# Optimization experiments

Measured on AMD Instinct MI355X. Metric: run time of the kernel, lower is better.

Reference implementation:

```python
import jax, jax.numpy as jnp
import numpy as np

B, C, T = 16, 256, 2048
K = 1024  # codes per layer
N_LAYERS = 3


def setup_inputs() -> dict:
    key = jax.random.key(0)
    kx, k0, k1, k2 = jax.random.split(key, 4)
    x = jax.random.normal(kx, (B, C, T), dtype=jnp.float32)
    scale = 1.0 / K
    emb0 = jax.random.uniform(k0, (K, C), minval=-scale, maxval=scale, dtype=jnp.float32)
    emb1 = jax.random.uniform(k1, (K, C), minval=-scale, maxval=scale, dtype=jnp.float32)
    emb2 = jax.random.uniform(k2, (K, C), minval=-scale, maxval=scale, dtype=jnp.float32)
    return {"x": x, "emb0": emb0, "emb1": emb1, "emb2": emb2}


def _vq_layer(x, emb):
    # x: [B, C, T], emb: [K, C]
    b, c, t = x.shape
    flat = jnp.transpose(x, (0, 2, 1)).reshape(-1, c)          # [B*T, C]
    # squared L2 distance to each code: ||f||^2 - 2 f.e + ||e||^2
    dist = (jnp.sum(flat * flat, axis=1, keepdims=True)
            - 2.0 * flat @ emb.T
            + jnp.sum(emb * emb, axis=1))                       # [B*T, K]
    idx = jnp.argmin(dist, axis=1)                              # [B*T]
    quant = jnp.transpose(emb[idx].reshape(b, t, c), (0, 2, 1)) # [B, C, T]
    sg = jax.lax.stop_gradient
    loss = jnp.mean((sg(quant) - x) ** 2) + jnp.mean((quant - sg(x)) ** 2)
    quantized = x + sg(quant - x)  # straight-through
    return quantized, loss


def reference(x, emb0, emb1, emb2):
    total_loss = jnp.float32(0.0)
    out = x
    for emb in (emb0, emb1, emb2):
        out, loss = _vq_layer(out, emb)
        total_loss = total_loss + loss
    return out, total_loss
```

## Files before the change

kernel.cpp:

```cpp
#include <hip/hip_runtime.h>
#include <stdint.h>

#define B_  16
#define C_  256
#define T_  2048
#define K_  1024
#define TOTAL_ELEMS 8388608

typedef short bf16x8 __attribute__((ext_vector_type(8)));
typedef float f32x4 __attribute__((ext_vector_type(4)));

__device__ __forceinline__ unsigned long long pack_key(float d, int idx) {
  unsigned u = __float_as_uint(d);
  u = (u & 0x80000000u) ? ~u : (u | 0x80000000u);
  return ((unsigned long long)u << 32) | (unsigned)idx;
}
__device__ __forceinline__ float unpack_dist(unsigned long long key) {
  unsigned du = (unsigned)(key >> 32);
  unsigned bits = (du & 0x80000000u) ? (du ^ 0x80000000u) : ~du;
  return __uint_as_float(bits);
}

__device__ __forceinline__ unsigned short f2bf_rne(float f) {
  unsigned u = __float_as_uint(f);
  unsigned r = u + 0x7FFFu + ((u >> 16) & 1u);
  return (unsigned short)(r >> 16);
}

__device__ __forceinline__ void gload_lds16(const void* g, void* l) {
  __builtin_amdgcn_global_load_lds(
      (const __attribute__((address_space(1))) unsigned int*)g,
      (__attribute__((address_space(3))) unsigned int*)l, 16, 0, 0);
}

__global__ __launch_bounds__(256) void prep_kernel(
    const float* __restrict__ e0, const float* __restrict__ e1,
    const float* __restrict__ e2, float* __restrict__ nrm,
    unsigned short* __restrict__ ebf) {
  int bid = blockIdx.x;
  if (bid < 12) {
    int i = bid * 256 + threadIdx.x;
    const float* e = (i < 1024) ? e0 : (i < 2048) ? e1 : e2;
    const float* p = e + (size_t)(i & 1023) * C_;
    float s = 0.0f;
    for (int c = 0; c < C_; c += 4) {
      float4 v = *(const float4*)(p + c);
      s = fmaf(v.x, v.x, s); s = fmaf(v.y, v.y, s);
      s = fmaf(v.z, v.z, s); s = fmaf(v.w, v.w, s);
    }
    nrm[i] = s;
  } else {
    int i = (bid - 12) * 256 + threadIdx.x;
    float4 v = *(const float4*)(e0 + (size_t)i * 4);
    unsigned lo = (unsigned)f2bf_rne(v.x) | ((unsigned)f2bf_rne(v.y) << 16);
    unsigned hi = (unsigned)f2bf_rne(v.z) | ((unsigned)f2bf_rne(v.w) << 16);
    *(uint2*)(ebf + (size_t)i * 4) = make_uint2(lo, hi);
  }
}

__global__ __launch_bounds__(256) void xpose_kernel(
    const float* __restrict__ x, unsigned short* __restrict__ xT) {
  __shared__ float ftile[64][68];
  int tid = threadIdx.x;
  int bid = blockIdx.x;
  int b  = bid >> 7;
  int t0 = ((bid >> 2) & 31) << 6;
  int c0 = (bid & 3) << 6;
  int w = tid >> 6, l = tid & 63;
  int c_loc = w * 16 + (l >> 4);
  int t_loc = (l & 15) * 4;
  const float* src = x + (size_t)b * (C_ * T_) + (size_t)(c0 + c_loc) * T_ + t0 + t_loc;
  float4 v = *(const float4*)src;
  *(float4*)&ftile[c_loc][t_loc] = v;
  __syncthreads();
  int t_row = tid >> 2;
  int cs = (tid & 3) * 16;
  unsigned pk[8];
#pragma unroll
  for (int i = 0; i < 8; i++) {
    unsigned short lo = f2bf_rne(ftile[cs + 2 * i][t_row]);
    unsigned short hi = f2bf_rne(ftile[cs + 2 * i + 1][t_row]);
    pk[i] = (unsigned)lo | ((unsigned)hi << 16);
  }
  unsigned short* dst = xT + ((size_t)(b * T_ + t0 + t_row) * C_ + c0 + cs);
  *(uint4*)dst       = make_uint4(pk[0], pk[1], pk[2], pk[3]);
  *((uint4*)dst + 1) = make_uint4(pk[4], pk[5], pk[6], pk[7]);
}

__global__ __launch_bounds__(256) void map_tile_kernel(
    const float* __restrict__ e0, const float* __restrict__ e1,
    const float* __restrict__ e2, const float* __restrict__ nrm,
    unsigned long long* __restrict__ keysM) {
  __shared__ float As[16][68];
  __shared__ float Bs[16][68];
  int bid = blockIdx.x;
  int m = bid >> 8;
  int tb = bid & 255;
  int ar0 = (tb >> 4) << 6;
  int br0 = (tb & 15) << 6;
  const float* Ap = m ? e1 : e0;
  const float* Bp = m ? e2 : e1;
  const float* nB = nrm + (m + 1) * 1024;

  int tid = threadIdx.x;
  int ty = tid >> 4, tx = tid & 15;
  int srow = tid >> 2;
  int skp  = (tid & 3) << 2;

  float acc[4][4];
#pragma unroll
  for (int i = 0; i < 4; i++)
#pragma unroll
    for (int j = 0; j < 4; j++) acc[i][j] = 0.0f;

  const float* gA = Ap + (size_t)(ar0 + srow) * C_ + skp;
  const float* gB = Bp + (size_t)(br0 + srow) * C_ + skp;

  for (int kk = 0; kk < C_; kk += 16) {
    float4 av = *(const float4*)(gA + kk);
    float4 bv = *(const float4*)(gB + kk);
    __syncthreads();
    As[skp + 0][srow] = av.x; As[skp + 1][srow] = av.y;
    As[skp + 2][srow] = av.z; As[skp + 3][srow] = av.w;
    Bs[skp + 0][srow] = bv.x; Bs[skp + 1][srow] = bv.y;
    Bs[skp + 2][srow] = bv.z; Bs[skp + 3][srow] = bv.w;
    __syncthreads();
#pragma unroll
    for (int k = 0; k < 16; k++) {
      float4 a4 = *(const float4*)&As[k][ty * 4];
      float4 b4 = *(const float4*)&Bs[k][tx * 4];
      float aa[4] = {a4.x, a4.y, a4.z, a4.w};
      float bb[4] = {b4.x, b4.y, b4.z, b4.w};
#pragma unroll
      for (int i = 0; i < 4; i++)
#pragma unroll
        for (int j = 0; j < 4; j++)
          acc[i][j] = fmaf(aa[i], bb[j], acc[i][j]);
    }
  }

  float nv[4];
#pragma unroll
  for (int j = 0; j < 4; j++) nv[j] = nB[br0 + tx * 4 + j];

#pragma unroll
  for (int i = 0; i < 4; i++) {
    unsigned long long best = 0xFFFFFFFFFFFFFFFFULL;
#pragma unroll
    for (int j = 0; j < 4; j++) {
      int code = br0 + tx * 4 + j;
      float s = nv[j] - 2.0f * acc[i][j];
      unsigned long long key = pack_key(s, code);
      if (key < best) best = key;
    }
#pragma unroll
    for (int off = 1; off < 16; off <<= 1) {
      unsigned long long o = __shfl_xor(best, off, 64);
      if (o < best) best = o;
    }
    if (tx == 0)
      atomicMin(&keysM[m * 1024 + ar0 + ty * 4 + i], best);
  }
}

__global__ __launch_bounds__(256) void l0_mfma_kernel(
    const unsigned short* __restrict__ xT, const unsigned short* __restrict__ ebf,
    const float* __restrict__ e0n, unsigned long long* __restrict__ keys) {
  __shared__ __align__(16) unsigned short AB[2][2][128][32];
  __shared__ unsigned long long kred[128][2];

  int tid = threadIdx.x;
  int l = tid & 63, w = tid >> 6;
  int wr = w >> 1, wc = w & 1;
  int mb = blockIdx.x & 255, nb = blockIdx.x >> 8;
  int row0 = mb << 7, kb = nb << 7;

  int sm = w * 32 + (l >> 2);
  int ks = (l & 3) ^ ((l >> 2) & 3);
  const unsigned short* gA = xT + ((size_t)(row0 + sm) * C_ + ks * 8);
  const unsigned short* gB = ebf + ((size_t)(kb + sm) * C_ + ks * 8);

  f32x4 acc[4][4];
#pragma unroll
  for (int mi = 0; mi < 4; mi++)
#pragma unroll
    for (int ni = 0; ni < 4; ni++) acc[mi][ni] = (f32x4){0.f, 0.f, 0.f, 0.f};

#define STAGE(buf, kk) do {                                              \
    char* baseA = (char*)&AB[(buf)][0][0][0] + w * 2048;                 \
    char* baseB = (char*)&AB[(buf)][1][0][0] + w * 2048;                 \
    gload_lds16(gA + (size_t)(kk) * 32, baseA);                          \
    gload_lds16(gA + (size_t)16 * C_ + (size_t)(kk) * 32, baseA + 1024); \
    gload_lds16(gB + (size_t)(kk) * 32, baseB);                          \
    gload_lds16(gB + (size_t)16 * C_ + (size_t)(kk) * 32, baseB + 1024); \
  } while (0)

  STAGE(0, 0);
  __syncthreads();

  int lr = l & 15, lg = l >> 4;
  int slot = lg ^ (lr & 3);
  int buf = 0;
  for (int kk = 0; kk < 8; kk++) {
    if (kk < 7) STAGE(buf ^ 1, kk + 1);
    bf16x8 aF[4], bF[4];
#pragma unroll
    for (int mi = 0; mi < 4; mi++)
      aF[mi] = *(const bf16x8*)&AB[buf][0][wr * 64 + mi * 16 + lr][slot * 8];
#pragma unroll
    for (int ni = 0; ni < 4; ni++)
      bF[ni] = *(const bf16x8*)&AB[buf][1][wc * 64 + ni * 16 + lr][slot * 8];
#pragma unroll
    for (int mi = 0; mi < 4; mi++)
#pragma unroll
      for (int ni = 0; ni < 4; ni++)
        acc[mi][ni] = __builtin_amdgcn_mfma_f32_16x16x32_bf16(
            aF[mi], bF[ni], acc[mi][ni], 0, 0, 0);
    __syncthreads();
    buf ^= 1;
  }
#undef STAGE

  float nv[4];
#pragma unroll
  for (int ni = 0; ni < 4; ni++) nv[ni] = e0n[kb + wc * 64 + ni * 16 + lr];

#pragma unroll
  for (int mi = 0; mi < 4; mi++) {
#pragma unroll
    for (int r = 0; r < 4; r++) {
      unsigned long long best = 0xFFFFFFFFFFFFFFFFULL;
#pragma unroll
      for (int ni = 0; ni < 4; ni++) {
        int code = kb + wc * 64 + ni * 16 + lr;
        float s = nv[ni] - 2.0f * acc[mi][ni][r];
        unsigned long long key = pack_key(s, code);
        if (key < best) best = key;
      }
#pragma unroll
      for (int off = 1; off < 16; off <<= 1) {
        unsigned long long o = __shfl_xor(best, off, 64);
        if (o < best) best = o;
      }
      if (lr == 0) kred[wr * 64 + mi * 16 + lg * 4 + r][wc] = best;
    }
  }
  __syncthreads();
  if (tid < 128) {
    unsigned long long b0 = kred[tid][0], b1 = kred[tid][1];
    atomicMin(&keys[row0 + tid], b0 < b1 ? b0 : b1);
  }
}

__global__ __launch_bounds__(256) void finish_kernel(
    const float* __restrict__ x, const float* __restrict__ emb2,
    const unsigned long long* __restrict__ keys,
    const unsigned long long* __restrict__ keysM,
    const float* __restrict__ nrm,
    float* __restrict__ out, float* __restrict__ loss_accum) {
  __shared__ int code2_l[64];
  __shared__ float rloss[64];
  __shared__ float fpart[4][64];
  int tid = threadIdx.x;
  int b  = blockIdx.x >> 5;
  int t0 = (blockIdx.x & 31) << 6;
  int tt = tid & 63, w = tid >> 6;

  if (w == 0) {
    unsigned long long key0 = keys[(size_t)b * T_ + t0 + tt];
    int idx0 = (int)(key0 & 0xFFFFFFFFULL);
    float s0 = unpack_dist(key0);
    unsigned long long k1 = keysM[idx0];
    int c1 = (int)(k1 & 0xFFFFFFFFULL);
    unsigned long long k2 = keysM[1024 + c1];
    code2_l[tt] = (int)(k2 & 0xFFFFFFFFULL);
    rloss[tt] = s0 + nrm[idx0] + unpack_dist(k1) + nrm[1024 + c1] + unpack_dist(k2);
  }
  __syncthreads();

  const float* xb = x + ((size_t)b << 19);
  float* ob = out + ((size_t)b << 19);
  int code2 = code2_l[tt];
  const float* e2row = emb2 + (size_t)code2 * C_;
  float fn = 0.0f;
  for (int c4 = w * 64; c4 < w * 64 + 64; c4 += 4) {
    float4 ev = *(const float4*)(e2row + c4);
    float evv[4] = {ev.x, ev.y, ev.z, ev.w};
#pragma unroll
    for (int u = 0; u < 4; u++) {
      size_t off = (size_t)(c4 + u) * T_ + t0 + tt;
      float v = xb[off];
      fn = fmaf(v, v, fn);
      ob[off] = evv[u];
    }
  }
  fpart[w][tt] = fn;
  __syncthreads();
  if (w == 0) {
    float tot = fpart[0][tt] + fpart[1][tt] + fpart[2][tt] + fpart[3][tt] + rloss[tt];
    for (int off = 32; off > 0; off >>= 1)
      tot += __shfl_down(tot, off, 64);
    if (tt == 0) atomicAdd(loss_accum, tot);
  }
}

__global__ void finalize_kernel(const float* __restrict__ loss_accum,
                                float* __restrict__ out_loss) {
  *out_loss = 2.0f * (*loss_accum) / 8388608.0f;
}

extern "C" void kernel_launch(void* const* d_in, const int* in_sizes, int n_in,
                              void* d_out, int out_size, void* d_ws, size_t ws_size,
                              hipStream_t stream) {
  const float* x  = (const float*)d_in[0];
  const float* e0 = (const float*)d_in[1];
  const float* e1 = (const float*)d_in[2];
  const float* e2 = (const float*)d_in[3];
  float* out = (float*)d_out;
  char* ws = (char*)d_ws;

  unsigned long long* keys  = (unsigned long long*)ws;
  unsigned long long* keysM = (unsigned long long*)(ws + 262144);
  float* nrm  = (float*)(ws + 278528);
  float* loss_accum = (float*)(ws + 290816);
  unsigned short* embbf = (unsigned short*)(ws + 294912);
  unsigned short* xT    = (unsigned short*)(ws + 819200);

  hipMemsetAsync(keys, 0xFF, 262144 + 16384, stream);
  hipMemsetAsync(loss_accum, 0, 4, stream);

  prep_kernel<<<268, 256, 0, stream>>>(e0, e1, e2, nrm, embbf);
  xpose_kernel<<<2048, 256, 0, stream>>>(x, xT);
  l0_mfma_kernel<<<2048, 256, 0, stream>>>(xT, embbf, nrm, keys);
  map_tile_kernel<<<512, 256, 0, stream>>>(e0, e1, e2, nrm, keysM);
  finish_kernel<<<512, 256, 0, stream>>>(x, e2, keys, keysM, nrm, out, loss_accum);
  finalize_kernel<<<1, 1, 0, stream>>>(loss_accum, out + TOTAL_ELEMS);
}
```

Before: 101.7 us.

## Fuse x-norm into transpose, fold memsets into prep, adjust LDS swizzle

Computes the sum of squares of x inside the transpose kernel, which already reads x, so the finish kernel no longer re-reads all of x. The memsets for keys and the loss accumulator move into extra blocks of the prep kernel to remove separate launches. The LDS swizzle pattern in the MFMA kernel changes to cut bank conflicts. This adds many atomics on one float address from the transpose blocks.

```diff
diff --git a/kernel.cpp b/kernel.cpp
--- a/kernel.cpp
+++ b/kernel.cpp
@@ -36,10 +36,12 @@
 __global__ __launch_bounds__(256) void prep_kernel(
     const float* __restrict__ e0, const float* __restrict__ e1,
     const float* __restrict__ e2, float* __restrict__ nrm,
-    unsigned short* __restrict__ ebf) {
+    unsigned short* __restrict__ ebf, uint4* __restrict__ keys_region,
+    float* __restrict__ loss_accum) {
   int bid = blockIdx.x;
+  int tid = threadIdx.x;
   if (bid < 12) {
-    int i = bid * 256 + threadIdx.x;
+    int i = bid * 256 + tid;
     const float* e = (i < 1024) ? e0 : (i < 2048) ? e1 : e2;
     const float* p = e + (size_t)(i & 1023) * C_;
     float s = 0.0f;
@@ -49,30 +51,47 @@
       s = fmaf(v.z, v.z, s); s = fmaf(v.w, v.w, s);
     }
     nrm[i] = s;
-  } else {
-    int i = (bid - 12) * 256 + threadIdx.x;
+  } else if (bid < 268) {
+    int i = (bid - 12) * 256 + tid;
     float4 v = *(const float4*)(e0 + (size_t)i * 4);
     unsigned lo = (unsigned)f2bf_rne(v.x) | ((unsigned)f2bf_rne(v.y) << 16);
     unsigned hi = (unsigned)f2bf_rne(v.z) | ((unsigned)f2bf_rne(v.w) << 16);
     *(uint2*)(ebf + (size_t)i * 4) = make_uint2(lo, hi);
+  } else {
+    int i = (bid - 268) * 256 + tid;
+    keys_region[i] = make_uint4(0xFFFFFFFFu, 0xFFFFFFFFu, 0xFFFFFFFFu, 0xFFFFFFFFu);
+    if (bid == 268 && tid == 0) *loss_accum = 0.0f;
   }
 }
 
 __global__ __launch_bounds__(256) void xpose_kernel(
-    const float* __restrict__ x, unsigned short* __restrict__ xT) {
+    const float* __restrict__ x, unsigned short* __restrict__ xT,
+    float* __restrict__ loss_accum) {
   __shared__ float ftile[64][68];
+  __shared__ float red[4];
   int tid = threadIdx.x;
   int bid = blockIdx.x;
   int b  = bid >> 7;
   int t0 = ((bid >> 2) & 31) << 6;
   int c0 = (bid & 3) << 6;
-  int w = tid >> 6, l = tid & 63;
-  int c_loc = w * 16 + (l >> 4);
-  int t_loc = (l & 15) * 4;
-  const float* src = x + (size_t)b * (C_ * T_) + (size_t)(c0 + c_loc) * T_ + t0 + t_loc;
-  float4 v = *(const float4*)src;
-  *(float4*)&ftile[c_loc][t_loc] = v;
+  int cr = tid >> 4;
+  int t_loc = (tid & 15) * 4;
+  const float* src = x + (size_t)b * (C_ * T_) + (size_t)c0 * T_ + t0;
+  float sq = 0.0f;
+#pragma unroll
+  for (int q = 0; q < 4; q++) {
+    int c_loc = cr + q * 16;
+    float4 v = *(const float4*)(src + (size_t)c_loc * T_ + t_loc);
+    *(float4*)&ftile[c_loc][t_loc] = v;
+    sq = fmaf(v.x, v.x, sq); sq = fmaf(v.y, v.y, sq);
+    sq = fmaf(v.z, v.z, sq); sq = fmaf(v.w, v.w, sq);
+  }
+  for (int off = 32; off > 0; off >>= 1) sq += __shfl_down(sq, off, 64);
+  if ((tid & 63) == 0) red[tid >> 6] = sq;
   __syncthreads();
+  if (tid == 0)
+    atomicAdd(loss_accum, red[0] + red[1] + red[2] + red[3]);
+
   int t_row = tid >> 2;
   int cs = (tid & 3) * 16;
   unsigned pk[8];
@@ -176,7 +195,7 @@
   int row0 = mb << 7, kb = nb << 7;
 
   int sm = w * 32 + (l >> 2);
-  int ks = (l & 3) ^ ((l >> 2) & 3);
+  int ks = (l & 3) ^ ((l >> 3) & 3);
   const unsigned short* gA = xT + ((size_t)(row0 + sm) * C_ + ks * 8);
   const unsigned short* gB = ebf + ((size_t)(kb + sm) * C_ + ks * 8);
 
@@ -199,7 +218,7 @@
   __syncthreads();
 
   int lr = l & 15, lg = l >> 4;
-  int slot = lg ^ (lr & 3);
+  int slot = lg ^ ((lr >> 1) & 3);
   int buf = 0;
   for (int kk = 0; kk < 8; kk++) {
     if (kk < 7) STAGE(buf ^ 1, kk + 1);
@@ -253,14 +272,13 @@
 }
 
 __global__ __launch_bounds__(256) void finish_kernel(
-    const float* __restrict__ x, const float* __restrict__ emb2,
+    const float* __restrict__ emb2,
     const unsigned long long* __restrict__ keys,
     const unsigned long long* __restrict__ keysM,
     const float* __restrict__ nrm,
     float* __restrict__ out, float* __restrict__ loss_accum) {
   __shared__ int code2_l[64];
   __shared__ float rloss[64];
-  __shared__ float fpart[4][64];
   int tid = threadIdx.x;
   int b  = blockIdx.x >> 5;
   int t0 = (blockIdx.x & 31) << 6;
@@ -278,26 +296,18 @@
   }
   __syncthreads();
 
-  const float* xb = x + ((size_t)b << 19);
   float* ob = out + ((size_t)b << 19);
   int code2 = code2_l[tt];
   const float* e2row = emb2 + (size_t)code2 * C_;
-  float fn = 0.0f;
   for (int c4 = w * 64; c4 < w * 64 + 64; c4 += 4) {
     float4 ev = *(const float4*)(e2row + c4);
     float evv[4] = {ev.x, ev.y, ev.z, ev.w};
 #pragma unroll
-    for (int u = 0; u < 4; u++) {
-      size_t off = (size_t)(c4 + u) * T_ + t0 + tt;
-      float v = xb[off];
-      fn = fmaf(v, v, fn);
-      ob[off] = evv[u];
-    }
-  }
-  fpart[w][tt] = fn;
-  __syncthreads();
+    for (int u = 0; u < 4; u++)
+      ob[(size_t)(c4 + u) * T_ + t0 + tt] = evv[u];
+  }
   if (w == 0) {
-    float tot = fpart[0][tt] + fpart[1][tt] + fpart[2][tt] + fpart[3][tt] + rloss[tt];
+    float tot = rloss[tt];
     for (int off = 32; off > 0; off >>= 1)
       tot += __shfl_down(tot, off, 64);
     if (tt == 0) atomicAdd(loss_accum, tot);
@@ -326,13 +336,10 @@
   unsigned short* embbf = (unsigned short*)(ws + 294912);
   unsigned short* xT    = (unsigned short*)(ws + 819200);
 
-  hipMemsetAsync(keys, 0xFF, 262144 + 16384, stream);
-  hipMemsetAsync(loss_accum, 0, 4, stream);
-
-  prep_kernel<<<268, 256, 0, stream>>>(e0, e1, e2, nrm, embbf);
-  xpose_kernel<<<2048, 256, 0, stream>>>(x, xT);
+  prep_kernel<<<336, 256, 0, stream>>>(e0, e1, e2, nrm, embbf, (uint4*)ws, loss_accum);
+  xpose_kernel<<<2048, 256, 0, stream>>>(x, xT, loss_accum);
   l0_mfma_kernel<<<2048, 256, 0, stream>>>(xT, embbf, nrm, keys);
   map_tile_kernel<<<512, 256, 0, stream>>>(e0, e1, e2, nrm, keysM);
-  finish_kernel<<<512, 256, 0, stream>>>(x, e2, keys, keysM, nrm, out, loss_accum);
+  finish_kernel<<<512, 256, 0, stream>>>(e2, keys, keysM, nrm, out, loss_accum);
   finalize_kernel<<<1, 1, 0, stream>>>(loss_accum, out + TOTAL_ELEMS);
 }
```

Result: slower. 115.4 us (+13.5%).
